# Performance work log

Measured on AMD Instinct MI355X. Metric: run time of the kernel, lower is better.

Reference implementation:

```python
import jax, jax.numpy as jnp
import numpy as np

NUM_CLASSES = 81
N_ROIS = 100000
N_GT = 512
ROIS_PER_IMAGE = 256
FG_ROIS_PER_IMAGE = 128  # fg_fraction * rois_per_image
FG_THRESH = 0.5
BG_HI = 0.5
BG_LO = 0.1


def _make_boxes(key, n, img=1024.0):
    k1, k2, k3, k4 = jax.random.split(key, 4)
    x1 = jax.random.uniform(k1, (n,)) * (img - 160.0)
    y1 = jax.random.uniform(k2, (n,)) * (img - 160.0)
    w = 16.0 + jax.random.uniform(k3, (n,)) * 112.0
    h = 16.0 + jax.random.uniform(k4, (n,)) * 112.0
    return jnp.stack([x1, y1, x1 + w, y1 + h], axis=1)


def setup_inputs() -> dict:
    key = jax.random.key(0)
    kg, kc, kn, kr, ks = jax.random.split(key, 5)
    gt_xyxy = _make_boxes(kg, N_GT)
    gt_cls = jax.random.randint(kc, (N_GT, 1), 1, NUM_CLASSES).astype(jnp.float32)
    gt_boxes = jnp.concatenate([gt_xyxy, gt_cls], axis=1)
    # first block of proposals = jittered gt boxes so fg samples exist
    n_jit = 4096
    reps = int(np.ceil(n_jit / N_GT))
    jit_base = jnp.tile(gt_xyxy, (reps, 1))[:n_jit]
    noise = (jax.random.uniform(kn, (n_jit, 4)) - 0.5) * 12.0
    jit_boxes = jit_base + noise
    rand_boxes = _make_boxes(kr, N_ROIS - n_jit)
    boxes = jnp.concatenate([jit_boxes, rand_boxes], axis=0)
    rpn_rois = jnp.concatenate([jnp.zeros((N_ROIS, 1), jnp.float32), boxes], axis=1)
    rpn_scores = jax.random.uniform(ks, (N_ROIS, 1), dtype=jnp.float32)
    return {"rpn_rois": rpn_rois, "rpn_scores": rpn_scores, "gt_boxes": gt_boxes}


def _bbox_overlaps(b1, b2):
    # b1 [N,4], b2 [G,4] -> IoU [N,G] with +1 pixel convention
    x1a, y1a, x2a, y2a = b1[:, 0], b1[:, 1], b1[:, 2], b1[:, 3]
    x1b, y1b, x2b, y2b = b2[:, 0], b2[:, 1], b2[:, 2], b2[:, 3]
    iw = jnp.maximum(0.0, jnp.minimum(x2a[:, None], x2b[None, :]) - jnp.maximum(x1a[:, None], x1b[None, :]) + 1.0)
    ih = jnp.maximum(0.0, jnp.minimum(y2a[:, None], y2b[None, :]) - jnp.maximum(y1a[:, None], y1b[None, :]) + 1.0)
    inter = iw * ih
    a1 = (x2a - x1a + 1.0) * (y2a - y1a + 1.0)
    a2 = (x2b - x1b + 1.0) * (y2b - y1b + 1.0)
    union = a1[:, None] + a2[None, :] - inter
    return jnp.where(inter == 0.0, 0.0, inter / union)


def _bbox_transform(ex, gt):
    ew = ex[:, 2] - ex[:, 0] + 1.0
    eh = ex[:, 3] - ex[:, 1] + 1.0
    ecx = ex[:, 0] + 0.5 * ew
    ecy = ex[:, 1] + 0.5 * eh
    gw = gt[:, 2] - gt[:, 0] + 1.0
    gh = gt[:, 3] - gt[:, 1] + 1.0
    gcx = gt[:, 0] + 0.5 * gw
    gcy = gt[:, 1] + 0.5 * gh
    return jnp.stack([(gcx - ecx) / ew, (gcy - ecy) / eh, jnp.log(gw / ew), jnp.log(gh / eh)], axis=1)


def _forward(rpn_rois, rpn_scores, gt_boxes):
    means = jnp.array([0.0, 0.0, 0.0, 0.0], jnp.float32)
    stds = jnp.array([0.1, 0.1, 0.2, 0.2], jnp.float32)
    k1, k2, k3 = jax.random.split(jax.random.key(42), 3)
    n = rpn_rois.shape[0]
    overlaps = _bbox_overlaps(rpn_rois[:, 1:5], gt_boxes[:, :4])  # [N,G]
    gt_assignment = jnp.argmax(overlaps, axis=1)  # [N]
    max_overlaps = jnp.max(overlaps, axis=1)      # [N]
    fg_mask = max_overlaps >= FG_THRESH
    bg_mask = (max_overlaps < BG_HI) & (max_overlaps >= BG_LO)
    # shuffled candidate orderings: random key for candidates, +2 sentinel pushes rest to the back
    fg_order = jnp.argsort(jnp.where(fg_mask, jax.random.uniform(k1, (n,)), 2.0))
    bg_order = jnp.argsort(jnp.where(bg_mask, jax.random.uniform(k2, (n,)), 2.0))
    fg_count = jnp.minimum(FG_ROIS_PER_IMAGE, jnp.sum(fg_mask))
    bg_count = jnp.minimum(ROIS_PER_IMAGE - fg_count, jnp.sum(bg_mask))
    pos = jnp.arange(ROIS_PER_IMAGE)
    sel = jnp.where(pos < fg_count, fg_order[pos], bg_order[jnp.maximum(pos - fg_count, 0)])
    # fill any shortfall by re-sampling uniformly from the fg+bg picks
    n_samp = fg_count + bg_count
    n_safe = jnp.maximum(n_samp, 1)
    dup = (jax.random.uniform(k3, (ROIS_PER_IMAGE,)) * n_safe).astype(jnp.int32)
    sel = jnp.where(pos < n_samp, sel, sel[dup])
    gt_ids = gt_assignment[sel]
    labels = gt_boxes[gt_ids, 4]
    fmax = max_overlaps[sel]
    labels = jnp.where((fmax < BG_HI) & (fmax >= BG_LO), 0.0, labels)
    rois = rpn_rois[sel]                 # [256,5]
    roi_scores = rpn_scores[sel].reshape(-1)
    targets = _bbox_transform(rois[:, 1:5], gt_boxes[gt_ids, :4])
    targets = (targets - means) / stds
    # expand compact (cls,tx,ty,tw,th) into N x 4K, nonzero only at own-class slot
    cls = labels.astype(jnp.int32)
    valid = (labels > 0).astype(jnp.float32)[:, None]
    rows = pos[:, None]
    cols = cls[:, None] * 4 + jnp.arange(4)[None, :]
    zeros4k = jnp.zeros((ROIS_PER_IMAGE, 4 * NUM_CLASSES), jnp.float32)
    bbox_targets = zeros4k.at[rows, cols].set(targets * valid)
    bbox_inside = zeros4k.at[rows, cols].set(jnp.ones((1, 4), jnp.float32) * valid)
    bbox_outside = (bbox_inside > 0).astype(jnp.float32)
    return rois, roi_scores, labels, bbox_targets, bbox_inside, bbox_outside


def reference(rpn_rois, rpn_scores, gt_boxes):
    return _forward(rpn_rois, rpn_scores, gt_boxes)
```

## Files before the change

kernel.cpp:

```cpp
#include <hip/hip_runtime.h>
#include <stdint.h>

__host__ __device__ inline void tf2x32(uint32_t ks0, uint32_t ks1, uint32_t x0, uint32_t x1,
                                       uint32_t& o0, uint32_t& o1) {
  uint32_t ks2 = ks0 ^ ks1 ^ 0x1BD11BDAu;
#define TFR(r) { x0 += x1; x1 = (x1 << (r)) | (x1 >> (32 - (r))); x1 ^= x0; }
  x0 += ks0; x1 += ks1;
  TFR(13) TFR(15) TFR(26) TFR(6)
  x0 += ks1; x1 += ks2 + 1u;
  TFR(17) TFR(29) TFR(16) TFR(24)
  x0 += ks2; x1 += ks0 + 2u;
  TFR(13) TFR(15) TFR(26) TFR(6)
  x0 += ks0; x1 += ks1 + 3u;
  TFR(17) TFR(29) TFR(16) TFR(24)
  x0 += ks1; x1 += ks2 + 4u;
  TFR(13) TFR(15) TFR(26) TFR(6)
  x0 += ks2; x1 += ks0 + 5u;
#undef TFR
  o0 = x0; o1 = x1;
}

__device__ inline float bits_to_unif(uint32_t b) {
  return __uint_as_float((b >> 9) | 0x3F800000u) - 1.0f;
}

__device__ inline uint32_t jbits(int v, uint32_t ka, uint32_t kb, uint32_t i, uint32_t n) {
  uint32_t o0, o1;
  if (v == 2) {
    uint32_t h = (n + 1) >> 1;
    if (i < h) {
      uint32_t xh = (i + h < n) ? (i + h) : 0u;
      tf2x32(ka, kb, i, xh, o0, o1);
      return o0;
    }
    tf2x32(ka, kb, i - h, i, o0, o1);
    return o1;
  }
  tf2x32(ka, kb, 0u, i, o0, o1);
  return (v == 0) ? o0 : (o0 ^ o1);
}

__device__ inline int jbucket(uint32_t b) { return (int)(b >> 22); }

#define NGT_MAX      512
#define ROIS_PER_IMG 256
#define FG_PER_IMG   128
#define NCOLS        324
#define NB           1024
#define CAND_CAP     2048
#define WAVES        4

#define OFF_SCORES 1280
#define OFF_LABELS 1536
#define OFF_BIG    1792
#define BIGN       (ROIS_PER_IMG * NCOLS)

#define WS_MAXOV   0
#define WS_GTASGN  400000
#define WS_HIST    800000
#define WS_CANDF   808192
#define WS_CANDB   824576
#define WS_META    840960
#define WS_CLS     841024
#define WS_T       842048

__global__ void __launch_bounds__(1024) k_detect(const float* __restrict__ scores,
                                                 int n,
                                                 int* __restrict__ meta,
                                                 int* __restrict__ hist) {
  int tid = threadIdx.x;
  hist[tid] = 0;
  hist[NB + tid] = 0;
  if (tid >= 7 && tid <= 13) meta[tid] = 0;

  if (tid < 64) {
    uint32_t pa, pb; tf2x32(0u, 0u, 0u, 4u, pa, pb);
    uint32_t t0, t1, q0, q1;
    tf2x32(0u, 0u, 3u, 8u, t0, t1);
    tf2x32(0u, 0u, 4u, 9u, q0, q1);
    uint32_t la = t1, lb = q1;

    bool m0 = false, m1 = false, m2 = false;
    if (tid < 16) {
      uint32_t sref = __float_as_uint(scores[tid]);
      uint32_t o0, o1; tf2x32(pa, pb, 0u, (uint32_t)tid, o0, o1);
      m0 = (__float_as_uint(bits_to_unif(o0)) == sref);
      m1 = (__float_as_uint(bits_to_unif(o0 ^ o1)) == sref);
      uint32_t h = (uint32_t)(n >> 1);
      uint32_t c0, c1; tf2x32(la, lb, (uint32_t)tid, (uint32_t)tid + h, c0, c1);
      m2 = (__float_as_uint(bits_to_unif(c0)) == sref);
    }
    int n0 = __popcll(__ballot(m0));
    int n1 = __popcll(__ballot(m1));
    int n2 = __popcll(__ballot(m2));
    if (tid == 0) {
      int v = (n1 >= n0 && n1 >= n2) ? 1 : ((n0 >= n2) ? 0 : 2);
      meta[0] = v;
      uint32_t K[6];
      if (v == 2) {
        uint32_t a0, a1, b0, b1, c0, c1;
        tf2x32(0u, 42u, 0u, 3u, a0, a1);
        tf2x32(0u, 42u, 1u, 4u, b0, b1);
        tf2x32(0u, 42u, 2u, 5u, c0, c1);
        K[0] = a0; K[1] = b0; K[2] = c0; K[3] = a1; K[4] = b1; K[5] = c1;
      } else {
        tf2x32(0u, 42u, 0u, 0u, K[0], K[1]);
        tf2x32(0u, 42u, 0u, 1u, K[2], K[3]);
        tf2x32(0u, 42u, 0u, 2u, K[4], K[5]);
      }
      for (int j = 0; j < 6; ++j) meta[1 + j] = (int)K[j];
    }
  }
}

__global__ void __launch_bounds__(256) k_iou(const float* __restrict__ rois,
                                             const float* __restrict__ gt,
                                             int n, int ngt,
                                             float* __restrict__ maxov,
                                             int* __restrict__ gtasgn,
                                             int* __restrict__ hist,
                                             const int* __restrict__ meta) {
#pragma clang fp contract(off)
  __shared__ float4 sgt4[NGT_MAX];
  __shared__ float sarea[NGT_MAX];
  __shared__ float sbest[WAVES][64];
  __shared__ int   sbi[WAVES][64];
  __shared__ int   smeta[7];
  const int tid = threadIdx.x;
  const int wave = tid >> 6;
  const int lane = tid & 63;
  if (tid < 7) smeta[tid] = meta[tid];
  for (int g = tid; g < ngt; g += blockDim.x) {
    float x1 = gt[g * 5 + 0], y1 = gt[g * 5 + 1];
    float x2 = gt[g * 5 + 2], y2 = gt[g * 5 + 3];
    sgt4[g] = make_float4(x1, y1, x2, y2);
    sarea[g] = (x2 - x1 + 1.0f) * (y2 - y1 + 1.0f);
  }
  __syncthreads();

  const int i = blockIdx.x * 64 + lane;
  const bool valid = (i < n);

  float ax1 = 1e30f, ay1 = 1e30f, ax2 = -1e30f, ay2 = -1e30f, a1 = 1.0f;
  if (valid) {
    ax1 = rois[i * 5 + 1]; ay1 = rois[i * 5 + 2];
    ax2 = rois[i * 5 + 3]; ay2 = rois[i * 5 + 4];
    a1 = (ax2 - ax1 + 1.0f) * (ay2 - ay1 + 1.0f);
  }

  const int csz = (ngt + WAVES - 1) / WAVES;
  const int g0 = wave * csz;
  const int cnt = max(0, min(ngt, g0 + csz) - g0);

  unsigned long long m0 = 0ull, m1 = 0ull;
  if (cnt == 128) {
#pragma unroll 8
    for (int jj = 0; jj < 64; ++jj) {
      float4 G = sgt4[g0 + jj];
      float iw = fminf(ax2, G.z) - fmaxf(ax1, G.x) + 1.0f;
      float ih = fminf(ay2, G.w) - fmaxf(ay1, G.y) + 1.0f;
      if (iw > 0.0f && ih > 0.0f) m0 |= (1ull << jj);
    }
#pragma unroll 8
    for (int jj = 0; jj < 64; ++jj) {
      float4 G = sgt4[g0 + 64 + jj];
      float iw = fminf(ax2, G.z) - fmaxf(ax1, G.x) + 1.0f;
      float ih = fminf(ay2, G.w) - fmaxf(ay1, G.y) + 1.0f;
      if (iw > 0.0f && ih > 0.0f) m1 |= (1ull << jj);
    }
  } else {
    const int c0 = min(cnt, 64);
    for (int jj = 0; jj < c0; ++jj) {
      float4 G = sgt4[g0 + jj];
      float iw = fminf(ax2, G.z) - fmaxf(ax1, G.x) + 1.0f;
      float ih = fminf(ay2, G.w) - fmaxf(ay1, G.y) + 1.0f;
      if (iw > 0.0f && ih > 0.0f) m0 |= (1ull << jj);
    }
    for (int jj = 64; jj < cnt; ++jj) {
      float4 G = sgt4[g0 + jj];
      float iw = fminf(ax2, G.z) - fmaxf(ax1, G.x) + 1.0f;
      float ih = fminf(ay2, G.w) - fmaxf(ay1, G.y) + 1.0f;
      if (iw > 0.0f && ih > 0.0f) m1 |= (1ull << (jj - 64));
    }
  }

  float best = 0.0f; int bi = 0;
  while (m0) {
    int jj = __builtin_ctzll(m0);
    m0 &= m0 - 1ull;
    int j = g0 + jj;
    float4 G = sgt4[j];
    float iw = fminf(ax2, G.z) - fmaxf(ax1, G.x) + 1.0f;
    float ih = fminf(ay2, G.w) - fmaxf(ay1, G.y) + 1.0f;
    float inter = iw * ih;
    float uni = a1 + sarea[j] - inter;
    float iou = inter / uni;
    if (iou > best) { best = iou; bi = j; }
  }
  while (m1) {
    int jj = __builtin_ctzll(m1);
    m1 &= m1 - 1ull;
    int j = g0 + 64 + jj;
    float4 G = sgt4[j];
    float iw = fminf(ax2, G.z) - fmaxf(ax1, G.x) + 1.0f;
    float ih = fminf(ay2, G.w) - fmaxf(ay1, G.y) + 1.0f;
    float inter = iw * ih;
    float uni = a1 + sarea[j] - inter;
    float iou = inter / uni;
    if (iou > best) { best = iou; bi = j; }
  }
  sbest[wave][lane] = best;
  sbi[wave][lane] = bi;
  __syncthreads();

  if (wave == 0 && valid) {
    for (int w = 1; w < WAVES; ++w) {
      float ob = sbest[w][lane];
      int oi = sbi[w][lane];
      if (ob > best || (ob == best && oi < bi)) { best = ob; bi = oi; }
    }
    maxov[i] = best;
    gtasgn[i] = bi;
    if (best >= 0.1f) {
      const int v = smeta[0];
      const bool fg = (best >= 0.5f);
      uint32_t ka = (uint32_t)(fg ? smeta[1] : smeta[3]);
      uint32_t kb = (uint32_t)(fg ? smeta[2] : smeta[4]);
      uint32_t b = jbits(v, ka, kb, (uint32_t)i, (uint32_t)n);
      atomicAdd(&hist[(fg ? 0 : NB) + jbucket(b)], 1);
    }
  }
}

__global__ void __launch_bounds__(1024) k_scan(const int* __restrict__ hist,
                                               int* __restrict__ meta) {
  __shared__ int hf[NB], hb[NB];
  const int tid = threadIdx.x;
  hf[tid] = hist[tid];
  hb[tid] = hist[NB + tid];
  __syncthreads();
  for (int s = 1; s < NB; s <<= 1) {
    int tf_ = hf[tid] + ((tid >= s) ? hf[tid - s] : 0);
    int tb_ = hb[tid] + ((tid >= s) ? hb[tid - s] : 0);
    __syncthreads();
    hf[tid] = tf_; hb[tid] = tb_;
    __syncthreads();
  }
  const int fg_count = min(FG_PER_IMG, hf[NB - 1]);
  const int bg_count = min(ROIS_PER_IMG - fg_count, hb[NB - 1]);
  if (tid == 0) {
    meta[9] = fg_count;
    meta[10] = bg_count;
    if (fg_count == 0) meta[7] = -1;
    if (bg_count == 0) meta[8] = -1;
  }
  if (fg_count > 0 && hf[tid] >= fg_count && (tid == 0 || hf[tid - 1] < fg_count)) meta[7] = tid;
  if (bg_count > 0 && hb[tid] >= bg_count && (tid == 0 || hb[tid - 1] < bg_count)) meta[8] = tid;
}

__global__ void k_collect(const float* __restrict__ maxov, int n,
                          int* __restrict__ meta,
                          unsigned long long* __restrict__ candf,
                          unsigned long long* __restrict__ candb) {
  __shared__ int smeta[9];
  if (threadIdx.x < 9) smeta[threadIdx.x] = meta[threadIdx.x];
  __syncthreads();
  const int i = blockIdx.x * blockDim.x + threadIdx.x;
  if (i >= n) return;
  const int v = smeta[0];
  const int Bf = smeta[7], Bb = smeta[8];
  float m = maxov[i];
  if (m >= 0.5f) {
    if (Bf >= 0) {
      uint32_t b = jbits(v, (uint32_t)smeta[1], (uint32_t)smeta[2], (uint32_t)i, (uint32_t)n);
      if (jbucket(b) <= Bf) {
        int p = atomicAdd(&meta[11], 1);
        if (p < CAND_CAP) candf[p] = ((unsigned long long)(b >> 9) << 32) | (unsigned)i;
      }
    }
  } else if (m >= 0.1f) {
    if (Bb >= 0) {
      uint32_t b = jbits(v, (uint32_t)smeta[3], (uint32_t)smeta[4], (uint32_t)i, (uint32_t)n);
      if (jbucket(b) <= Bb) {
        int p = atomicAdd(&meta[12], 1);
        if (p < CAND_CAP) candb[p] = ((unsigned long long)(b >> 9) << 32) | (unsigned)i;
      }
    }
  }
}

__device__ inline void bitonic(unsigned long long* buf, int nelem, int tid, int nthr) {
  for (int k = 2; k <= nelem; k <<= 1)
    for (int j = k >> 1; j > 0; j >>= 1) {
      for (int i = tid; i < nelem; i += nthr) {
        int l = i ^ j;
        if (l > i) {
          unsigned long long a = buf[i], b = buf[l];
          bool swap_ = ((i & k) == 0) ? (a > b) : (a < b);
          if (swap_) { buf[i] = b; buf[l] = a; }
        }
      }
      __syncthreads();
    }
}

__global__ void __launch_bounds__(1024) k_pick(
    const float* __restrict__ rois, const float* __restrict__ scores,
    const float* __restrict__ gt,
    const float* __restrict__ maxov, const int* __restrict__ gtasgn,
    const int* __restrict__ meta,
    const unsigned long long* __restrict__ gcandf,
    const unsigned long long* __restrict__ gcandb,
    float* __restrict__ out, int* __restrict__ ws_cls, float* __restrict__ ws_t) {
#pragma clang fp contract(off)
  __shared__ unsigned long long candf[CAND_CAP], candb[CAND_CAP];
  __shared__ int sel[ROIS_PER_IMG];
  __shared__ int smeta[13];
  const int tid = threadIdx.x;
  const int nthr = 1024;
  if (tid < 13) smeta[tid] = meta[tid];
  __syncthreads();
  const int v = smeta[0];
  const uint32_t k3a = (uint32_t)smeta[5], k3b = (uint32_t)smeta[6];
  const int fg_count = smeta[9], bg_count = smeta[10];
  const int Mf = min(smeta[11], CAND_CAP);
  const int Mb = min(smeta[12], CAND_CAP);

  int nf = 1; while (nf < Mf) nf <<= 1;
  int nb = 1; while (nb < Mb) nb <<= 1;
  for (int i = tid; i < nf; i += nthr) candf[i] = (i < Mf) ? gcandf[i] : ~0ull;
  for (int i = tid; i < nb; i += nthr) candb[i] = (i < Mb) ? gcandb[i] : ~0ull;
  __syncthreads();

  bitonic(candf, nf, tid, nthr);
  bitonic(candb, nb, tid, nthr);
  __syncthreads();

  if (tid < fg_count) sel[tid] = (int)(candf[tid] & 0xFFFFFFFFull);
  if (tid < bg_count) sel[fg_count + tid] = (int)(candb[tid] & 0xFFFFFFFFull);
  __syncthreads();

  const int n_samp = fg_count + bg_count;
  if (tid < ROIS_PER_IMG && tid >= n_samp) {
    if (n_samp > 0) {
      uint32_t b3 = jbits(v, k3a, k3b, (uint32_t)tid, (uint32_t)ROIS_PER_IMG);
      int d = (int)(bits_to_unif(b3) * (float)n_samp);
      d = min(d, n_samp - 1);
      sel[tid] = sel[d];
    } else {
      sel[tid] = 0;
    }
  }
  __syncthreads();

  if (tid < ROIS_PER_IMG) {
    int i = sel[tid];
    int g = gtasgn[i];
    float fmax = maxov[i];
    float label = gt[g * 5 + 4];
    if (fmax < 0.5f && fmax >= 0.1f) label = 0.0f;

    for (int c = 0; c < 5; ++c) out[tid * 5 + c] = rois[i * 5 + c];
    out[OFF_SCORES + tid] = scores[i];
    out[OFF_LABELS + tid] = label;

    float ex0 = rois[i * 5 + 1], ey0 = rois[i * 5 + 2];
    float ex1 = rois[i * 5 + 3], ey1 = rois[i * 5 + 4];
    float gx0 = gt[g * 5 + 0], gy0 = gt[g * 5 + 1];
    float gx1 = gt[g * 5 + 2], gy1 = gt[g * 5 + 3];
    float ew = ex1 - ex0 + 1.0f, eh = ey1 - ey0 + 1.0f;
    float ecx = ex0 + 0.5f * ew, ecy = ey0 + 0.5f * eh;
    float gw = gx1 - gx0 + 1.0f, gh = gy1 - gy0 + 1.0f;
    float gcx = gx0 + 0.5f * gw, gcy = gy0 + 0.5f * gh;
    float t0 = ((gcx - ecx) / ew) / 0.1f;
    float t1 = ((gcy - ecy) / eh) / 0.1f;
    float t2 = logf(gw / ew) / 0.2f;
    float t3 = logf(gh / eh) / 0.2f;

    float valid = (label > 0.0f) ? 1.0f : 0.0f;
    int cls = (int)label;
    ws_cls[tid] = (valid > 0.0f) ? cls : -1;
    ws_t[tid * 4 + 0] = t0 * valid;
    ws_t[tid * 4 + 1] = t1 * valid;
    ws_t[tid * 4 + 2] = t2 * valid;
    ws_t[tid * 4 + 3] = t3 * valid;
  }
}

__global__ void k_out(const int* __restrict__ ws_cls, const float* __restrict__ ws_t,
                      float* __restrict__ out) {
  int e = blockIdx.x * blockDim.x + threadIdx.x;
  if (e >= BIGN) return;
  int r = e / NCOLS, c = e % NCOLS;
  int cls = ws_cls[r];
  float tv = 0.0f, iv = 0.0f;
  if (cls >= 0) {
    int c0 = cls * 4;
    if (c >= c0 && c < c0 + 4) { tv = ws_t[r * 4 + (c - c0)]; iv = 1.0f; }
  }
  out[OFF_BIG + e] = tv;
  out[OFF_BIG + BIGN + e] = iv;
  out[OFF_BIG + 2 * BIGN + e] = iv;
}

extern "C" void kernel_launch(void* const* d_in, const int* in_sizes, int n_in,
                              void* d_out, int out_size, void* d_ws, size_t ws_size,
                              hipStream_t stream) {
  const float* rois   = (const float*)d_in[0];
  const float* scores = (const float*)d_in[1];
  const float* gt     = (const float*)d_in[2];
  float* out = (float*)d_out;

  const int n   = in_sizes[0] / 5;
  const int ngt = in_sizes[2] / 5;

  char* ws = (char*)d_ws;
  float* maxov  = (float*)(ws + WS_MAXOV);
  int*   gtasgn = (int*)(ws + WS_GTASGN);
  int*   hist   = (int*)(ws + WS_HIST);
  unsigned long long* candf = (unsigned long long*)(ws + WS_CANDF);
  unsigned long long* candb = (unsigned long long*)(ws + WS_CANDB);
  int*   meta   = (int*)(ws + WS_META);
  int*   wcls   = (int*)(ws + WS_CLS);
  float* wt     = (float*)(ws + WS_T);

  k_detect<<<1, 1024, 0, stream>>>(scores, n, meta, hist);
  k_iou<<<(n + 63) / 64, 256, 0, stream>>>(rois, gt, n, ngt, maxov, gtasgn, hist, meta);
  k_scan<<<1, 1024, 0, stream>>>(hist, meta);
  k_collect<<<(n + 255) / 256, 256, 0, stream>>>(maxov, n, meta, candf, candb);
  k_pick<<<1, 1024, 0, stream>>>(rois, scores, gt, maxov, gtasgn, meta,
                                 candf, candb, out, wcls, wt);
  k_out<<<(BIGN + 255) / 256, 256, 0, stream>>>(wcls, wt, out);
}
```

Baseline: 71.04 us.

## Process two ROIs per lane in IoU kernel and pre-pack GT boxes

Each lane of the IoU kernel now handles two ROIs, so each shared-memory GT load is reused for twice the rows and the grid is halved. This amortizes the per-block GT staging into shared memory. The detect kernel now pre-packs GT boxes with precomputed areas into an aligned 8-float layout, so the IoU blocks load them as float4 instead of strided scalars. The overlap test is also simplified to compare against -1 rather than adding 1. In exchange there is higher register pressure and fewer blocks, which may reduce occupancy and latency hiding.

Measured after the change: 73.64 us. 3.7% more time.

```diff
diff --git a/kernel.cpp b/kernel.cpp
--- a/kernel.cpp
+++ b/kernel.cpp
@@ -63,15 +63,29 @@
 #define WS_META    840960
 #define WS_CLS     841024
 #define WS_T       842048
+#define WS_GT8     846144
 
 __global__ void __launch_bounds__(1024) k_detect(const float* __restrict__ scores,
-                                                 int n,
+                                                 const float* __restrict__ gt,
+                                                 int n, int ngt,
                                                  int* __restrict__ meta,
-                                                 int* __restrict__ hist) {
+                                                 int* __restrict__ hist,
+                                                 float* __restrict__ gt8) {
+#pragma clang fp contract(off)
   int tid = threadIdx.x;
   hist[tid] = 0;
   hist[NB + tid] = 0;
   if (tid >= 7 && tid <= 13) meta[tid] = 0;
+
+  if (tid < NGT_MAX && tid < ngt) {
+    float x1 = gt[tid * 5 + 0], y1 = gt[tid * 5 + 1];
+    float x2 = gt[tid * 5 + 2], y2 = gt[tid * 5 + 3];
+    gt8[tid * 8 + 0] = x1; gt8[tid * 8 + 1] = y1;
+    gt8[tid * 8 + 2] = x2; gt8[tid * 8 + 3] = y2;
+    gt8[tid * 8 + 4] = (x2 - x1 + 1.0f) * (y2 - y1 + 1.0f);
+    gt8[tid * 8 + 5] = gt[tid * 5 + 4];
+    gt8[tid * 8 + 6] = 0.0f; gt8[tid * 8 + 7] = 0.0f;
+  }
 
   if (tid < 64) {
     uint32_t pa, pb; tf2x32(0u, 0u, 0u, 4u, pa, pb);
@@ -114,7 +128,7 @@
 }
 
 __global__ void __launch_bounds__(256) k_iou(const float* __restrict__ rois,
-                                             const float* __restrict__ gt,
+                                             const float* __restrict__ gt8,
                                              int n, int ngt,
                                              float* __restrict__ maxov,
                                              int* __restrict__ gtasgn,
@@ -123,111 +137,132 @@
 #pragma clang fp contract(off)
   __shared__ float4 sgt4[NGT_MAX];
   __shared__ float sarea[NGT_MAX];
-  __shared__ float sbest[WAVES][64];
-  __shared__ int   sbi[WAVES][64];
+  __shared__ float sbest[WAVES][128];
+  __shared__ int   sbi[WAVES][128];
   __shared__ int   smeta[7];
   const int tid = threadIdx.x;
   const int wave = tid >> 6;
   const int lane = tid & 63;
   if (tid < 7) smeta[tid] = meta[tid];
-  for (int g = tid; g < ngt; g += blockDim.x) {
-    float x1 = gt[g * 5 + 0], y1 = gt[g * 5 + 1];
-    float x2 = gt[g * 5 + 2], y2 = gt[g * 5 + 3];
-    sgt4[g] = make_float4(x1, y1, x2, y2);
-    sarea[g] = (x2 - x1 + 1.0f) * (y2 - y1 + 1.0f);
-  }
-  __syncthreads();
-
-  const int i = blockIdx.x * 64 + lane;
-  const bool valid = (i < n);
-
-  float ax1 = 1e30f, ay1 = 1e30f, ax2 = -1e30f, ay2 = -1e30f, a1 = 1.0f;
-  if (valid) {
-    ax1 = rois[i * 5 + 1]; ay1 = rois[i * 5 + 2];
-    ax2 = rois[i * 5 + 3]; ay2 = rois[i * 5 + 4];
-    a1 = (ax2 - ax1 + 1.0f) * (ay2 - ay1 + 1.0f);
+  {
+    const float4* g4p = (const float4*)gt8;
+    for (int g = tid; g < ngt; g += 256) {
+      float4 box = g4p[2 * g];
+      float4 ext = g4p[2 * g + 1];
+      sgt4[g] = box;
+      sarea[g] = ext.x;
+    }
+  }
+  __syncthreads();
+
+  const int R = blockIdx.x * 128;
+  const int iA = R + lane;
+  const int iB = R + lane + 64;
+  const bool pA = (iA < n), pB = (iB < n);
+
+  float ax1 = 1e30f, ay1 = 1e30f, ax2 = -1e30f, ay2 = -1e30f, a1A = 1.0f;
+  float bx1 = 1e30f, by1 = 1e30f, bx2 = -1e30f, by2 = -1e30f, a1B = 1.0f;
+  if (pA) {
+    ax1 = rois[iA * 5 + 1]; ay1 = rois[iA * 5 + 2];
+    ax2 = rois[iA * 5 + 3]; ay2 = rois[iA * 5 + 4];
+    a1A = (ax2 - ax1 + 1.0f) * (ay2 - ay1 + 1.0f);
+  }
+  if (pB) {
+    bx1 = rois[iB * 5 + 1]; by1 = rois[iB * 5 + 2];
+    bx2 = rois[iB * 5 + 3]; by2 = rois[iB * 5 + 4];
+    a1B = (bx2 - bx1 + 1.0f) * (by2 - by1 + 1.0f);
   }
 
   const int csz = (ngt + WAVES - 1) / WAVES;
   const int g0 = wave * csz;
   const int cnt = max(0, min(ngt, g0 + csz) - g0);
 
-  unsigned long long m0 = 0ull, m1 = 0ull;
+  unsigned long long mA0 = 0ull, mA1 = 0ull, mB0 = 0ull, mB1 = 0ull;
   if (cnt == 128) {
 #pragma unroll 8
     for (int jj = 0; jj < 64; ++jj) {
       float4 G = sgt4[g0 + jj];
-      float iw = fminf(ax2, G.z) - fmaxf(ax1, G.x) + 1.0f;
-      float ih = fminf(ay2, G.w) - fmaxf(ay1, G.y) + 1.0f;
-      if (iw > 0.0f && ih > 0.0f) m0 |= (1ull << jj);
+      bool oA = (fminf(ax2, G.z) - fmaxf(ax1, G.x) > -1.0f) &&
+                (fminf(ay2, G.w) - fmaxf(ay1, G.y) > -1.0f);
+      bool oB = (fminf(bx2, G.z) - fmaxf(bx1, G.x) > -1.0f) &&
+                (fminf(by2, G.w) - fmaxf(by1, G.y) > -1.0f);
+      if (oA) mA0 |= (1ull << jj);
+      if (oB) mB0 |= (1ull << jj);
     }
 #pragma unroll 8
     for (int jj = 0; jj < 64; ++jj) {
       float4 G = sgt4[g0 + 64 + jj];
-      float iw = fminf(ax2, G.z) - fmaxf(ax1, G.x) + 1.0f;
-      float ih = fminf(ay2, G.w) - fmaxf(ay1, G.y) + 1.0f;
-      if (iw > 0.0f && ih > 0.0f) m1 |= (1ull << jj);
+      bool oA = (fminf(ax2, G.z) - fmaxf(ax1, G.x) > -1.0f) &&
+                (fminf(ay2, G.w) - fmaxf(ay1, G.y) > -1.0f);
+      bool oB = (fminf(bx2, G.z) - fmaxf(bx1, G.x) > -1.0f) &&
+                (fminf(by2, G.w) - fmaxf(by1, G.y) > -1.0f);
+      if (oA) mA1 |= (1ull << jj);
+      if (oB) mB1 |= (1ull << jj);
     }
   } else {
-    const int c0 = min(cnt, 64);
-    for (int jj = 0; jj < c0; ++jj) {
+    for (int jj = 0; jj < cnt; ++jj) {
       float4 G = sgt4[g0 + jj];
-      float iw = fminf(ax2, G.z) - fmaxf(ax1, G.x) + 1.0f;
-      float ih = fminf(ay2, G.w) - fmaxf(ay1, G.y) + 1.0f;
-      if (iw > 0.0f && ih > 0.0f) m0 |= (1ull << jj);
-    }
-    for (int jj = 64; jj < cnt; ++jj) {
-      float4 G = sgt4[g0 + jj];
-      float iw = fminf(ax2, G.z) - fmaxf(ax1, G.x) + 1.0f;
-      float ih = fminf(ay2, G.w) - fmaxf(ay1, G.y) + 1.0f;
-      if (iw > 0.0f && ih > 0.0f) m1 |= (1ull << (jj - 64));
-    }
-  }
-
-  float best = 0.0f; int bi = 0;
-  while (m0) {
-    int jj = __builtin_ctzll(m0);
-    m0 &= m0 - 1ull;
-    int j = g0 + jj;
-    float4 G = sgt4[j];
-    float iw = fminf(ax2, G.z) - fmaxf(ax1, G.x) + 1.0f;
-    float ih = fminf(ay2, G.w) - fmaxf(ay1, G.y) + 1.0f;
-    float inter = iw * ih;
-    float uni = a1 + sarea[j] - inter;
-    float iou = inter / uni;
-    if (iou > best) { best = iou; bi = j; }
-  }
-  while (m1) {
-    int jj = __builtin_ctzll(m1);
-    m1 &= m1 - 1ull;
-    int j = g0 + 64 + jj;
-    float4 G = sgt4[j];
-    float iw = fminf(ax2, G.z) - fmaxf(ax1, G.x) + 1.0f;
-    float ih = fminf(ay2, G.w) - fmaxf(ay1, G.y) + 1.0f;
-    float inter = iw * ih;
-    float uni = a1 + sarea[j] - inter;
-    float iou = inter / uni;
-    if (iou > best) { best = iou; bi = j; }
-  }
-  sbest[wave][lane] = best;
-  sbi[wave][lane] = bi;
-  __syncthreads();
-
-  if (wave == 0 && valid) {
+      bool oA = (fminf(ax2, G.z) - fmaxf(ax1, G.x) > -1.0f) &&
+                (fminf(ay2, G.w) - fmaxf(ay1, G.y) > -1.0f);
+      bool oB = (fminf(bx2, G.z) - fmaxf(bx1, G.x) > -1.0f) &&
+                (fminf(by2, G.w) - fmaxf(by1, G.y) > -1.0f);
+      if (jj < 64) {
+        if (oA) mA0 |= (1ull << jj);
+        if (oB) mB0 |= (1ull << jj);
+      } else {
+        if (oA) mA1 |= (1ull << (jj - 64));
+        if (oB) mB1 |= (1ull << (jj - 64));
+      }
+    }
+  }
+
+  float bestA = 0.0f, bestB = 0.0f;
+  int biA = 0, biB = 0;
+  auto drain = [&](unsigned long long m, int base,
+                   float x1r, float y1r, float x2r, float y2r, float a1r,
+                   float& best, int& bi) {
+    while (m) {
+      int jj = __builtin_ctzll(m);
+      m &= m - 1ull;
+      int j = base + jj;
+      float4 G = sgt4[j];
+      float iw = fminf(x2r, G.z) - fmaxf(x1r, G.x) + 1.0f;
+      float ih = fminf(y2r, G.w) - fmaxf(y1r, G.y) + 1.0f;
+      float inter = iw * ih;
+      float uni = a1r + sarea[j] - inter;
+      float iou = inter / uni;
+      if (iou > best) { best = iou; bi = j; }
+    }
+  };
+  drain(mA0, g0,      ax1, ay1, ax2, ay2, a1A, bestA, biA);
+  drain(mA1, g0 + 64, ax1, ay1, ax2, ay2, a1A, bestA, biA);
+  drain(mB0, g0,      bx1, by1, bx2, by2, a1B, bestB, biB);
+  drain(mB1, g0 + 64, bx1, by1, bx2, by2, a1B, bestB, biB);
+
+  sbest[wave][lane] = bestA;      sbi[wave][lane] = biA;
+  sbest[wave][lane + 64] = bestB; sbi[wave][lane + 64] = biB;
+  __syncthreads();
+
+  if (tid < 128) {
+    const int r = R + tid;
+    float best = sbest[0][tid];
+    int bi = sbi[0][tid];
     for (int w = 1; w < WAVES; ++w) {
-      float ob = sbest[w][lane];
-      int oi = sbi[w][lane];
+      float ob = sbest[w][tid];
+      int oi = sbi[w][tid];
       if (ob > best || (ob == best && oi < bi)) { best = ob; bi = oi; }
     }
-    maxov[i] = best;
-    gtasgn[i] = bi;
-    if (best >= 0.1f) {
-      const int v = smeta[0];
-      const bool fg = (best >= 0.5f);
-      uint32_t ka = (uint32_t)(fg ? smeta[1] : smeta[3]);
-      uint32_t kb = (uint32_t)(fg ? smeta[2] : smeta[4]);
-      uint32_t b = jbits(v, ka, kb, (uint32_t)i, (uint32_t)n);
-      atomicAdd(&hist[(fg ? 0 : NB) + jbucket(b)], 1);
+    if (r < n) {
+      maxov[r] = best;
+      gtasgn[r] = bi;
+      if (best >= 0.1f) {
+        const int v = smeta[0];
+        const bool fg = (best >= 0.5f);
+        uint32_t ka = (uint32_t)(fg ? smeta[1] : smeta[3]);
+        uint32_t kb = (uint32_t)(fg ? smeta[2] : smeta[4]);
+        uint32_t b = jbits(v, ka, kb, (uint32_t)r, (uint32_t)n);
+        atomicAdd(&hist[(fg ? 0 : NB) + jbucket(b)], 1);
+      }
     }
   }
 }
@@ -423,9 +458,10 @@
   int*   meta   = (int*)(ws + WS_META);
   int*   wcls   = (int*)(ws + WS_CLS);
   float* wt     = (float*)(ws + WS_T);
-
-  k_detect<<<1, 1024, 0, stream>>>(scores, n, meta, hist);
-  k_iou<<<(n + 63) / 64, 256, 0, stream>>>(rois, gt, n, ngt, maxov, gtasgn, hist, meta);
+  float* gt8    = (float*)(ws + WS_GT8);
+
+  k_detect<<<1, 1024, 0, stream>>>(scores, gt, n, ngt, meta, hist, gt8);
+  k_iou<<<(n + 127) / 128, 256, 0, stream>>>(rois, gt8, n, ngt, maxov, gtasgn, hist, meta);
   k_scan<<<1, 1024, 0, stream>>>(hist, meta);
   k_collect<<<(n + 255) / 256, 256, 0, stream>>>(maxov, n, meta, candf, candb);
   k_pick<<<1, 1024, 0, stream>>>(rois, scores, gt, maxov, gtasgn, meta,
```

## Fuse histogram scan into collect kernel and vectorize bbox output writes

Applied to the files above, without the earlier changes.

Removes the separate single-block scan launch: every 1024-thread collect block now redundantly recomputes the prefix scan over the histogram in shared memory to find the cutoff buckets, then filters its own slice. This drops one kernel launch and its serialization, at the cost of the scan work being repeated per block. Separately, the dense bbox output kernel now writes float4 per thread instead of scalars, with each thread deciding whether its quad is the class slot.

Measured after the change: 70.61 us. No clear change (-0.6%).

```diff
diff --git a/kernel.cpp b/kernel.cpp
--- a/kernel.cpp
+++ b/kernel.cpp
@@ -232,10 +232,18 @@
   }
 }
 
-__global__ void __launch_bounds__(1024) k_scan(const int* __restrict__ hist,
-                                               int* __restrict__ meta) {
+__global__ void __launch_bounds__(1024) k_collect(const float* __restrict__ maxov,
+                                                  int n,
+                                                  const int* __restrict__ hist,
+                                                  int* __restrict__ meta,
+                                                  unsigned long long* __restrict__ candf,
+                                                  unsigned long long* __restrict__ candb) {
   __shared__ int hf[NB], hb[NB];
+  __shared__ int smeta[7];
+  __shared__ int sres[2];
   const int tid = threadIdx.x;
+  if (tid < 7) smeta[tid] = meta[tid];
+  if (tid < 2) sres[tid] = -1;
   hf[tid] = hist[tid];
   hb[tid] = hist[NB + tid];
   __syncthreads();
@@ -246,29 +254,17 @@
     hf[tid] = tf_; hb[tid] = tb_;
     __syncthreads();
   }
-  const int fg_count = min(FG_PER_IMG, hf[NB - 1]);
-  const int bg_count = min(ROIS_PER_IMG - fg_count, hb[NB - 1]);
-  if (tid == 0) {
-    meta[9] = fg_count;
-    meta[10] = bg_count;
-    if (fg_count == 0) meta[7] = -1;
-    if (bg_count == 0) meta[8] = -1;
-  }
-  if (fg_count > 0 && hf[tid] >= fg_count && (tid == 0 || hf[tid - 1] < fg_count)) meta[7] = tid;
-  if (bg_count > 0 && hb[tid] >= bg_count && (tid == 0 || hb[tid - 1] < bg_count)) meta[8] = tid;
-}
-
-__global__ void k_collect(const float* __restrict__ maxov, int n,
-                          int* __restrict__ meta,
-                          unsigned long long* __restrict__ candf,
-                          unsigned long long* __restrict__ candb) {
-  __shared__ int smeta[9];
-  if (threadIdx.x < 9) smeta[threadIdx.x] = meta[threadIdx.x];
-  __syncthreads();
-  const int i = blockIdx.x * blockDim.x + threadIdx.x;
+  const int fgc = min(FG_PER_IMG, hf[NB - 1]);
+  const int bgc = min(ROIS_PER_IMG - fgc, hb[NB - 1]);
+  if (tid == 0) { meta[9] = fgc; meta[10] = bgc; }
+  if (fgc > 0 && hf[tid] >= fgc && (tid == 0 || hf[tid - 1] < fgc)) { sres[0] = tid; meta[7] = tid; }
+  if (bgc > 0 && hb[tid] >= bgc && (tid == 0 || hb[tid - 1] < bgc)) { sres[1] = tid; meta[8] = tid; }
+  __syncthreads();
+  const int Bf = sres[0], Bb = sres[1];
+  const int v = smeta[0];
+
+  const int i = blockIdx.x * 1024 + tid;
   if (i >= n) return;
-  const int v = smeta[0];
-  const int Bf = smeta[7], Bb = smeta[8];
   float m = maxov[i];
   if (m >= 0.5f) {
     if (Bf >= 0) {
@@ -389,18 +385,24 @@
 
 __global__ void k_out(const int* __restrict__ ws_cls, const float* __restrict__ ws_t,
                       float* __restrict__ out) {
-  int e = blockIdx.x * blockDim.x + threadIdx.x;
-  if (e >= BIGN) return;
-  int r = e / NCOLS, c = e % NCOLS;
+  const int QROW = NCOLS / 4;
+  const int TOT4 = ROIS_PER_IMG * QROW;
+  int e4 = blockIdx.x * blockDim.x + threadIdx.x;
+  if (e4 >= TOT4) return;
+  int r = e4 / QROW, q = e4 - r * QROW;
   int cls = ws_cls[r];
-  float tv = 0.0f, iv = 0.0f;
-  if (cls >= 0) {
-    int c0 = cls * 4;
-    if (c >= c0 && c < c0 + 4) { tv = ws_t[r * 4 + (c - c0)]; iv = 1.0f; }
-  }
-  out[OFF_BIG + e] = tv;
-  out[OFF_BIG + BIGN + e] = iv;
-  out[OFF_BIG + 2 * BIGN + e] = iv;
+  float4 tv = make_float4(0.f, 0.f, 0.f, 0.f);
+  float4 iv = make_float4(0.f, 0.f, 0.f, 0.f);
+  if (cls >= 0 && q == cls) {
+    tv = *(const float4*)(ws_t + r * 4);
+    iv = make_float4(1.f, 1.f, 1.f, 1.f);
+  }
+  float4* o0 = (float4*)(out + OFF_BIG);
+  float4* o1 = (float4*)(out + OFF_BIG + BIGN);
+  float4* o2 = (float4*)(out + OFF_BIG + 2 * BIGN);
+  o0[e4] = tv;
+  o1[e4] = iv;
+  o2[e4] = iv;
 }
 
 extern "C" void kernel_launch(void* const* d_in, const int* in_sizes, int n_in,
@@ -426,9 +428,8 @@
 
   k_detect<<<1, 1024, 0, stream>>>(scores, n, meta, hist);
   k_iou<<<(n + 63) / 64, 256, 0, stream>>>(rois, gt, n, ngt, maxov, gtasgn, hist, meta);
-  k_scan<<<1, 1024, 0, stream>>>(hist, meta);
-  k_collect<<<(n + 255) / 256, 256, 0, stream>>>(maxov, n, meta, candf, candb);
+  k_collect<<<(n + 1023) / 1024, 1024, 0, stream>>>(maxov, n, hist, meta, candf, candb);
   k_pick<<<1, 1024, 0, stream>>>(rois, scores, gt, maxov, gtasgn, meta,
                                  candf, candb, out, wcls, wt);
-  k_out<<<(BIGN + 255) / 256, 256, 0, stream>>>(wcls, wt, out);
-}
+  k_out<<<(ROIS_PER_IMG * (NCOLS / 4) + 255) / 256, 256, 0, stream>>>(wcls, wt, out);
+}
```
